# Kernel tuning notes

Measured on AMD Instinct MI355X. Metric: run time of the kernel, lower is better.

Reference implementation:

```python
import jax, jax.numpy as jnp
import numpy as np

# Irreps config: node = 64x0e + 32x1o, edge sh = 1x0e + 1x1o
N, E = 50000, 800000
MUL0, MUL1 = 64, 32
D_IN = MUL0 + 3 * MUL1          # 160
FC_H = 64
W_NUMEL = MUL0 + MUL0 + MUL1 + MUL1  # 192, per-instruction uvu weights
SQRT3 = 1.7320508075688772
ACT_C = 1.6791   # e3nn normalize2mom constant for silu


def setup_inputs() -> dict:
    key = jax.random.key(0)
    ks = jax.random.split(key, 11)
    return {
        "x": jax.random.normal(ks[0], (N, D_IN), jnp.float32),
        "edge_scalars": jax.random.uniform(ks[1], (E, FC_H), dtype=jnp.float32),
        "edge_attr_sh": jax.random.normal(ks[2], (E, 4), jnp.float32),
        "edge_index": jax.random.randint(ks[3], (2, E), 0, N),
        "w_fc1": jax.random.normal(ks[4], (FC_H, FC_H), jnp.float32),
        "w_fc2": jax.random.normal(ks[5], (FC_H, W_NUMEL), jnp.float32),
        "w_sc_s": jax.random.normal(ks[6], (MUL0, MUL0), jnp.float32),
        "w_sc_v": jax.random.normal(ks[7], (MUL1, MUL1), jnp.float32),
        "w_lin_s": jax.random.normal(ks[8], (96, MUL0), jnp.float32),
        "w_lin_v": jax.random.normal(ks[9], (96, MUL1), jnp.float32),
        "w_alpha": jax.random.normal(ks[10], (96, 1), jnp.float32) * 0.1,
    }


def reference(x, edge_scalars, edge_attr_sh, edge_index, w_fc1, w_fc2,
              w_sc_s, w_sc_v, w_lin_s, w_lin_v, w_alpha):
    src, dst = edge_index[0], edge_index[1]

    # --- fc: FullyConnectedNet([64, 64, 192], silu), e3nn fan-in norm ---
    h = jax.nn.silu(edge_scalars @ w_fc1 / np.sqrt(FC_H)) * ACT_C
    weight = h @ w_fc2 / np.sqrt(FC_H)                       # [E, 192]
    w0 = weight[:, :MUL0]                 # 0e x 0e -> 0e (mul 64)
    w1 = weight[:, MUL0:2 * MUL0]         # 0e x 1o -> 1o (mul 64)
    w2 = weight[:, 2 * MUL0:2 * MUL0 + MUL1]   # 1o x 0e -> 1o (mul 32)
    w3 = weight[:, 2 * MUL0 + MUL1:]           # 1o x 1o -> 0e (mul 32)

    # --- self connection: o3.Linear(in -> out), per-irrep mixing ---
    x_s = x[:, :MUL0]                                   # [N, 64]
    x_v = x[:, MUL0:].reshape(N, MUL1, 3)               # [N, 32, 3]
    sc_s = x_s @ w_sc_s / np.sqrt(MUL0)
    sc_v = jnp.einsum('nui,uw->nwi', x_v, w_sc_v) / np.sqrt(MUL1)
    sc_out = jnp.concatenate([sc_s, sc_v.reshape(N, 3 * MUL1)], axis=1)

    # --- gather + edge-weighted uvu tensor product ---
    gx_s = x_s[src]                                     # [E, 64]
    gx_v = x_v[src]                                     # [E, 32, 3]
    sh_s = edge_attr_sh[:, 0:1]                         # [E, 1]
    sh_v = edge_attr_sh[:, 1:4]                         # [E, 3]

    # path weights fold with w3j so factors cancel for 1o outputs
    mid_s0 = w0 * gx_s * sh_s                                        # [E,64] 0e
    mid_s1 = w3 * jnp.einsum('eui,ei->eu', gx_v, sh_v) / SQRT3       # [E,32] 0e
    mid_v0 = w1[:, :, None] * gx_s[:, :, None] * sh_v[:, None, :]    # [E,64,3] 1o
    mid_v1 = w2[:, :, None] * gx_v * sh_s[:, :, None]                # [E,32,3] 1o
    edge_feat = jnp.concatenate(
        [mid_s0, mid_s1, mid_v0.reshape(E, 3 * MUL0), mid_v1.reshape(E, 3 * MUL1)],
        axis=1)                                                      # [E, 384]

    # --- scatter-mean to destination nodes ---
    seg = jax.ops.segment_sum(edge_feat, dst, num_segments=N)
    cnt = jax.ops.segment_sum(jnp.ones((E,), edge_feat.dtype), dst, num_segments=N)
    mean = seg / jnp.maximum(cnt, 1.0)[:, None]                      # [N, 384]

    m_s = mean[:, :96]                                   # 96x0e
    m_v = mean[:, 96:].reshape(N, 96, 3)                 # 96x1o

    # --- alpha gate (o3.Linear mid -> 0e) and output linear ---
    alpha = m_s @ w_alpha / np.sqrt(96)                  # [N, 1]
    lin_s = m_s @ w_lin_s / np.sqrt(96)                  # [N, 64]
    lin_v = jnp.einsum('nui,uw->nwi', m_v, w_lin_v) / np.sqrt(96)
    lin_out = jnp.concatenate([lin_s, lin_v.reshape(N, 3 * MUL1)], axis=1)

    # sc.output_mask is all-ones here (every output irrep reachable)
    return sc_out + alpha * lin_out
```

## Files before the change

### kernel.cpp

```cpp
#include <hip/hip_runtime.h>

#define N_NODES 50000
#define N_EDGES 800000
#define MUL0 64
#define MUL1 32
#define D_IN 160
#define FC_H 64
#define W_NUMEL 192
#define FEAT 384
#define ACT_C 1.6791f
#define INV_SQRT3 0.57735026918962576f
#define RSQRT32 0.17677669529663687f
#define RSQRT96 0.10206207261596575f

#define TILE 32

typedef __attribute__((ext_vector_type(8))) short s16x8;
typedef __attribute__((ext_vector_type(4))) float f32x4;
typedef _Float16 h8 __attribute__((ext_vector_type(8)));
typedef __fp16 fp16x2 __attribute__((ext_vector_type(2)));

static __device__ __forceinline__ unsigned short f2bf(float f) {
    unsigned u = __builtin_bit_cast(unsigned, f);
    unsigned r = (u + 0x7fffu + ((u >> 16) & 1u)) >> 16;
    return (unsigned short)r;
}

static __device__ __forceinline__ int swz(int row, int byte_in_row) {
    int unit = ((row & 1) << 2) | (byte_in_row >> 4);
    int su = unit ^ ((row >> 1) & 7);
    return (row >> 1) * 128 + su * 16 + (byte_in_row & 15);
}
static __device__ __forceinline__ h8 rdh8(const unsigned char* base, int row, int eb) {
    return *(const h8*)(base + swz(row, eb));
}


__global__ __launch_bounds__(256) void hist_kernel(const int* __restrict__ eidx,
                                                   int* __restrict__ cnt) {
    int e = blockIdx.x * 256 + threadIdx.x;
    if (e < N_EDGES) atomicAdd(&cnt[eidx[N_EDGES + e]], 1);
}

#define SCAN_NB 64
#define SCAN_CH ((N_NODES + SCAN_NB - 1) / SCAN_NB)

__global__ __launch_bounds__(256) void scanA_kernel(const int* __restrict__ cnt,
                                                    int* __restrict__ bsum) {
    __shared__ int sred[4];
    int b = blockIdx.x, t = threadIdx.x;
    int lim = min((b + 1) * SCAN_CH, N_NODES);
    int s = 0;
    for (int i = b * SCAN_CH + t; i < lim; i += 256) s += cnt[i];
    for (int d = 1; d < 64; d <<= 1) s += __shfl_xor(s, d);
    if ((t & 63) == 0) sred[t >> 6] = s;
    __syncthreads();
    if (t == 0) bsum[b] = sred[0] + sred[1] + sred[2] + sred[3];
}

__global__ __launch_bounds__(64) void scanB_kernel(const int* __restrict__ bsum,
                                                   int* __restrict__ boff) {
    int t = threadIdx.x;
    int v = bsum[t];
    int p = v;
    for (int d = 1; d < 64; d <<= 1) { int u = __shfl_up(p, d); if (t >= d) p += u; }
    boff[t] = p - v;
}

__global__ __launch_bounds__(256) void scanC_kernel(const int* __restrict__ cnt,
                                                    const int* __restrict__ boff,
                                                    int* __restrict__ fill) {
    __shared__ int s_w[4];
    int b = blockIdx.x, t = threadIdx.x;
    const int CH2 = (SCAN_CH + 255) / 256;
    int base = b * SCAN_CH + t * CH2;
    int lim = min((b + 1) * SCAN_CH, N_NODES);
    int s = 0;
#pragma unroll
    for (int k = 0; k < CH2; ++k) { int i = base + k; if (i < lim) s += cnt[i]; }
    int v = s;
    for (int d = 1; d < 64; d <<= 1) { int u = __shfl_up(v, d); if ((t & 63) >= d) v += u; }
    if ((t & 63) == 63) s_w[t >> 6] = v;
    __syncthreads();
    if (t == 0) { int run = 0; for (int w = 0; w < 4; ++w) { int tv = s_w[w]; s_w[w] = run; run += tv; } }
    __syncthreads();
    int run = boff[b] + s_w[t >> 6] + (v - s);
#pragma unroll
    for (int k = 0; k < CH2; ++k) {
        int i = base + k;
        if (i < lim) { fill[i] = run; run += cnt[i]; }
    }
}

__global__ __launch_bounds__(256) void scatter_ids_kernel(const int* __restrict__ eidx,
                                                          int* __restrict__ fill,
                                                          int* __restrict__ sorted_eid) {
    int e = blockIdx.x * 256 + threadIdx.x;
    if (e < N_EDGES) {
        int p = atomicAdd(&fill[eidx[N_EDGES + e]], 1);
        sorted_eid[p] = e;
    }
}

__global__ __launch_bounds__(256) void prep_w_kernel(
    const float* __restrict__ w_fc1,
    const float* __restrict__ w_fc2,
    const float* __restrict__ w_sc_s,
    const float* __restrict__ w_sc_v,
    const float* __restrict__ w_lin_s,
    const float* __restrict__ w_lin_v,
    unsigned short* __restrict__ w1t,
    unsigned short* __restrict__ w2t,
    unsigned short* __restrict__ wscs_t,
    unsigned short* __restrict__ wscv_t,
    unsigned short* __restrict__ wlins_t,
    unsigned short* __restrict__ wlinv_t)
{
    int i = blockIdx.x * 256 + threadIdx.x;
    if (i < 64 * 64)  w1t[i]    = f2bf(w_fc1[(i & 63) * FC_H + (i >> 6)]);
    if (i < 192 * 64) w2t[i]    = f2bf(w_fc2[(i & 63) * W_NUMEL + (i >> 6)]);
    if (i < 64 * 64)  wscs_t[i] = f2bf(w_sc_s[(i & 63) * 64 + (i >> 6)]);
    if (i < 32 * 32)  wscv_t[i] = f2bf(w_sc_v[(i & 31) * 32 + (i >> 5)]);
    if (i < 64 * 96)  wlins_t[i] = f2bf(w_lin_s[(i % 96) * 64 + (i / 96)]);
    if (i < 32 * 96)  wlinv_t[i] = f2bf(w_lin_v[(i % 96) * 32 + (i / 96)]);
}

#define X_OFF    0
#define W_OFF    10240
#define SH_OFF   22528
#define SID_OFF  22784
#define SEGN_OFF 22848
#define NSEG_OFF 22976
#define SMEM_SZ  22980

static __device__ __forceinline__ h8 seg_mask(const unsigned* vv, unsigned tgt) {
    h8 a;
#pragma unroll
    for (int w2 = 0; w2 < 4; ++w2) {
        a[w2 * 2]     = ((vv[w2] & 0xffffu) == tgt) ? (_Float16)1.f : (_Float16)0.f;
        a[w2 * 2 + 1] = ((vv[w2] >> 16)     == tgt) ? (_Float16)1.f : (_Float16)0.f;
    }
    return a;
}

__global__ __launch_bounds__(256) void edge_kernel(
    const float* __restrict__ x,
    const float* __restrict__ es,
    const float* __restrict__ sh,
    const int*   __restrict__ eidx,
    const int*   __restrict__ sorted_eid,
    const unsigned short* __restrict__ w1t,
    const unsigned short* __restrict__ w2t,
    float* __restrict__ accg)
{
    __shared__ __align__(16) unsigned char smem[SMEM_SZ];
    int* s_segnode = (int*)(smem + SEGN_OFF);
    unsigned short* s_sid = (unsigned short*)(smem + SID_OFF);

    const int t = threadIdx.x;
    const int l = t & 63;
    const int wv = t >> 6;
    const int lr = l & 15;
    const int lk = l >> 4;
    const int rg   = wv & 1;
    const int half = wv >> 1;
    const int tile0 = blockIdx.x * TILE;

    s16x8 w1b[2][2];
#pragma unroll
    for (int j = 0; j < 2; ++j)
#pragma unroll
        for (int kk = 0; kk < 2; ++kk)
            w1b[j][kk] = *(const s16x8*)(w1t + ((half * 2 + j) * 16 + lr) * 64 + kk * 32 + lk * 8);

    int eid_own = sorted_eid[tile0 + rg * 16 + lr];
    float4 esf[4];
    {
        const float4* ep = (const float4*)(es + (size_t)eid_own * FC_H);
        esf[0] = ep[lk * 2];     esf[1] = ep[lk * 2 + 1];
        esf[2] = ep[8 + lk * 2]; esf[3] = ep[8 + lk * 2 + 1];
    }
    const int xe = l & 31;
    const int xc0 = (wv * 2 + (l >> 5)) * 5;
    const int src_e = eidx[sorted_eid[tile0 + xe]];
    float4 xg[5];
    {
        const float4* xp = (const float4*)(x + (size_t)src_e * D_IN);
#pragma unroll
        for (int k = 0; k < 5; ++k) xg[k] = xp[xc0 + k];
    }
    float shv = 0.f;
    if (t < 128) shv = sh[(size_t)sorted_eid[tile0 + (t >> 2)] * 4 + (t & 3)];
    if (wv == 0) {
        int dl = (l < 32) ? eidx[N_EDGES + sorted_eid[tile0 + l]] : -1;
        int nd = __shfl_down(dl, 1);
        bool flag = (l == 31) || (l < 31 && dl != nd);
        unsigned long long m = __ballot(flag) & 0xffffffffull;
        int sid = __popcll(m & ((1ull << l) - 1ull));
        if (l < 32) {
            s_sid[l] = (unsigned short)sid;
            if (flag) s_segnode[sid] = dl;
            if (l == 31) *(int*)(smem + NSEG_OFF) = sid + 1;
        }
    }

    unsigned short* s_h = (unsigned short*)(smem + X_OFF);
    s16x8 afrag[2];
    {
        s16x8 a;
        a[0] = f2bf(esf[0].x); a[1] = f2bf(esf[0].y); a[2] = f2bf(esf[0].z); a[3] = f2bf(esf[0].w);
        a[4] = f2bf(esf[1].x); a[5] = f2bf(esf[1].y); a[6] = f2bf(esf[1].z); a[7] = f2bf(esf[1].w);
        afrag[0] = a;
        a[0] = f2bf(esf[2].x); a[1] = f2bf(esf[2].y); a[2] = f2bf(esf[2].z); a[3] = f2bf(esf[2].w);
        a[4] = f2bf(esf[3].x); a[5] = f2bf(esf[3].y); a[6] = f2bf(esf[3].z); a[7] = f2bf(esf[3].w);
        afrag[1] = a;
    }
#pragma unroll
    for (int j = 0; j < 2; ++j) {
        int nt = half * 2 + j;
        f32x4 hacc = {0.f, 0.f, 0.f, 0.f};
#pragma unroll
        for (int kk = 0; kk < 2; ++kk)
            hacc = __builtin_amdgcn_mfma_f32_16x16x32_bf16(afrag[kk], w1b[j][kk], hacc, 0, 0, 0);
#pragma unroll
        for (int q = 0; q < 4; ++q) {
            float aa = hacc[q] * 0.125f;
            float hv = aa * (1.f / (1.f + __expf(-aa))) * ACT_C;
            s_h[(rg * 16 + lk * 4 + q) * 72 + nt * 16 + lr] = f2bf(hv);
        }
    }
    __syncthreads();

    s16x8 hfrag[2];
#pragma unroll
    for (int kk = 0; kk < 2; ++kk)
        hfrag[kk] = *(const s16x8*)(s_h + (rg * 16 + lr) * 72 + kk * 32 + lk * 8);
    __syncthreads();

#pragma unroll
    for (int j = 0; j < 6; ++j) {
        int nt = half * 6 + j;
        f32x4 acc = {0.f, 0.f, 0.f, 0.f};
#pragma unroll
        for (int kk = 0; kk < 2; ++kk) {
            s16x8 b = *(const s16x8*)(w2t + (nt * 16 + lr) * 64 + kk * 32 + lk * 8);
            acc = __builtin_amdgcn_mfma_f32_16x16x32_bf16(hfrag[kk], b, acc, 0, 0, 0);
        }
        int f = nt * 16 + lr;
        fp16x2 p0 = __builtin_amdgcn_cvt_pkrtz(acc[0] * 0.125f, acc[1] * 0.125f);
        fp16x2 p1 = __builtin_amdgcn_cvt_pkrtz(acc[2] * 0.125f, acc[3] * 0.125f);
        uint2 wval = { __builtin_bit_cast(unsigned, p0), __builtin_bit_cast(unsigned, p1) };
        *(uint2*)(smem + W_OFF + swz(f, rg * 32 + lk * 8)) = wval;
    }
#pragma unroll
    for (int k = 0; k < 5; ++k) {
        float4 v = xg[k];
#pragma unroll
        for (int jj = 0; jj < 4; ++jj) {
            int r = (xc0 + k) * 4 + jj;
            float fv = (jj == 0) ? v.x : (jj == 1) ? v.y : (jj == 2) ? v.z : v.w;
            *(_Float16*)(smem + X_OFF + swz(r, xe * 2)) = (_Float16)fv;
        }
    }
    if (t < 128) {
        int e = t >> 2, c = t & 3;
        *(_Float16*)(smem + SH_OFF + swz(c, e * 2)) = (_Float16)shv;
    }
    __syncthreads();

    const int nseg = *(const int*)(smem + NSEG_OFF);
    const int eb = lk * 16;

    h8 shr[4];
#pragma unroll
    for (int r = 0; r < 4; ++r) shr[r] = rdh8(smem + SH_OFF, r, eb);
    uint4 sv = *(const uint4*)(smem + SID_OFF + eb);
    unsigned vv[4] = { sv.x, sv.y, sv.z, sv.w };

#pragma unroll
    for (int jj = 0; jj < 4; ++jj) {
        const int job = wv * 4 + jj;
        int cls, colbase;
        if (job < 4)       { cls = 0; colbase = job * 16; }
        else if (job < 10) { cls = 1; colbase = (job - 4) * 16; }
        else if (job < 14) { cls = 2; colbase = (job - 10) * 16; }
        else               { cls = 3; colbase = (job - 14) * 16; }
        const int col = colbase + lr;

        h8 B;
        if (cls == 0)      B = rdh8(smem + W_OFF, col, eb)        * rdh8(smem + X_OFF, col, eb);
        else if (cls == 1) B = rdh8(smem + W_OFF, 128 + col / 3, eb) * rdh8(smem + X_OFF, 64 + col, eb);
        else if (cls == 2) B = rdh8(smem + W_OFF, 64 + col, eb)   * rdh8(smem + X_OFF, col, eb);
        else {
            h8 d = rdh8(smem + X_OFF, 64 + 3 * col, eb)     * shr[1]
                 + rdh8(smem + X_OFF, 64 + 3 * col + 1, eb) * shr[2]
                 + rdh8(smem + X_OFF, 64 + 3 * col + 2, eb) * shr[3];
            B = rdh8(smem + W_OFF, 160 + col, eb) * d;
        }

        const int npass = (cls == 2) ? (3 * nseg + 15) >> 4 : (nseg + 15) >> 4;
        for (int p = 0; p < npass; ++p) {
            int m = p * 16 + lr;
            h8 A;
            if (cls == 2) {
                int sg = m / 3, i3 = m - 3 * sg;
                h8 shs = (i3 == 0) ? shr[1] : (i3 == 1) ? shr[2] : shr[3];
                A = seg_mask(vv, (unsigned)sg) * shs;
            } else if (cls == 3) {
                A = seg_mask(vv, (unsigned)m);
            } else {
                A = seg_mask(vv, (unsigned)m) * shr[0];
            }
            f32x4 acc = {0.f, 0.f, 0.f, 0.f};
            acc = __builtin_amdgcn_mfma_f32_16x16x32_f16(A, B, acc, 0, 0, 0);
#pragma unroll
            for (int q = 0; q < 4; ++q) {
                int mrow = p * 16 + lk * 4 + q;
                int sg, f; float sc = 1.f;
                if (cls == 0)      { sg = mrow; f = col; }
                else if (cls == 1) { sg = mrow; f = 288 + col; }
                else if (cls == 2) { sg = mrow / 3; f = 96 + 3 * col + (mrow - 3 * sg); }
                else               { sg = mrow; f = 64 + col; sc = INV_SQRT3; }
                if (sg < nseg) {
                    float val = acc[q] * sc;
                    float* addr = accg + (size_t)s_segnode[sg] * FEAT + f;
                    if (sg > 0 && sg < nseg - 1) *addr = val;
                    else atomicAdd(addr, val);
                }
            }
        }
    }
}


static __device__ __forceinline__ s16x8 frag_c8(const float* p, float s) {
    float4 u = *(const float4*)p, v = *(const float4*)(p + 4);
    s16x8 a;
    a[0] = f2bf(u.x * s); a[1] = f2bf(u.y * s); a[2] = f2bf(u.z * s); a[3] = f2bf(u.w * s);
    a[4] = f2bf(v.x * s); a[5] = f2bf(v.y * s); a[6] = f2bf(v.z * s); a[7] = f2bf(v.w * s);
    return a;
}

__global__ __launch_bounds__(256) void node_kernel(
    const float* __restrict__ x,
    const float* __restrict__ accg,
    const int*   __restrict__ cnt,
    const unsigned short* __restrict__ wscs_t,
    const unsigned short* __restrict__ wscv_t,
    const unsigned short* __restrict__ wlins_t,
    const unsigned short* __restrict__ wlinv_t,
    const float* __restrict__ w_alpha,
    float* __restrict__ out)
{
    const int t = threadIdx.x;
    const int wv = t >> 6, l = t & 63;
    const int lr = l & 15, lk = l >> 4;
    const int n_base = blockIdx.x * 64 + wv * 16;
    const int nrow = n_base + lr;
    const int nclamp = min(nrow, N_NODES - 1);

    const float* mrow = accg + (size_t)nclamp * FEAT;
    const float* xrow = x + (size_t)nclamp * D_IN;
    const float rinv = 1.f / (float)max(cnt[nclamp], 1);

    s16x8 ax[2], ams[3], axv[3], amv[3][3];
#pragma unroll
    for (int kk = 0; kk < 2; ++kk) ax[kk] = frag_c8(xrow + kk * 32 + lk * 8, 1.f);
#pragma unroll
    for (int kk = 0; kk < 3; ++kk) ams[kk] = frag_c8(mrow + kk * 32 + lk * 8, rinv);
    {
        float xb[24];
        const float4* p = (const float4*)(xrow + 64 + 24 * lk);
#pragma unroll
        for (int q = 0; q < 6; ++q) ((float4*)xb)[q] = p[q];
#pragma unroll
        for (int i = 0; i < 3; ++i) {
            s16x8 a;
#pragma unroll
            for (int j = 0; j < 8; ++j) a[j] = f2bf(xb[3 * j + i]);
            axv[i] = a;
        }
    }
#pragma unroll
    for (int kk = 0; kk < 3; ++kk) {
        float mb[24];
        const float4* p = (const float4*)(mrow + 96 + 96 * kk + 24 * lk);
#pragma unroll
        for (int q = 0; q < 6; ++q) ((float4*)mb)[q] = p[q];
#pragma unroll
        for (int i = 0; i < 3; ++i) {
            s16x8 a;
#pragma unroll
            for (int j = 0; j < 8; ++j) a[j] = f2bf(mb[3 * j + i] * rinv);
            amv[i][kk] = a;
        }
    }

    float ap = 0.f;
    {
        float ab[24];
        const float4* p = (const float4*)(mrow + 24 * lk);
#pragma unroll
        for (int q = 0; q < 6; ++q) ((float4*)ab)[q] = p[q];
#pragma unroll
        for (int j = 0; j < 24; ++j) ap += ab[j] * rinv * w_alpha[lk * 24 + j];
    }
    ap += __shfl_xor(ap, 16);
    ap += __shfl_xor(ap, 32);
    const float alphav = ap * RSQRT96;

    f32x4 accA[4], accL[4];
#pragma unroll
    for (int nt = 0; nt < 4; ++nt) { accA[nt] = (f32x4){0,0,0,0}; accL[nt] = (f32x4){0,0,0,0}; }
#pragma unroll
    for (int nt = 0; nt < 4; ++nt) {
#pragma unroll
        for (int kk = 0; kk < 2; ++kk) {
            s16x8 b = *(const s16x8*)(wscs_t + (nt * 16 + lr) * 64 + kk * 32 + lk * 8);
            accA[nt] = __builtin_amdgcn_mfma_f32_16x16x32_bf16(ax[kk], b, accA[nt], 0, 0, 0);
        }
#pragma unroll
        for (int kk = 0; kk < 3; ++kk) {
            s16x8 b = *(const s16x8*)(wlins_t + (nt * 16 + lr) * 96 + kk * 32 + lk * 8);
            accL[nt] = __builtin_amdgcn_mfma_f32_16x16x32_bf16(ams[kk], b, accL[nt], 0, 0, 0);
        }
    }
    f32x4 accVs[3][2], accVl[3][2];
#pragma unroll
    for (int i = 0; i < 3; ++i)
#pragma unroll
        for (int nt = 0; nt < 2; ++nt) { accVs[i][nt] = (f32x4){0,0,0,0}; accVl[i][nt] = (f32x4){0,0,0,0}; }
#pragma unroll
    for (int i = 0; i < 3; ++i) {
#pragma unroll
        for (int nt = 0; nt < 2; ++nt) {
            s16x8 b = *(const s16x8*)(wscv_t + (nt * 16 + lr) * 32 + lk * 8);
            accVs[i][nt] = __builtin_amdgcn_mfma_f32_16x16x32_bf16(axv[i], b, accVs[i][nt], 0, 0, 0);
#pragma unroll
            for (int kk = 0; kk < 3; ++kk) {
                s16x8 b2 = *(const s16x8*)(wlinv_t + (nt * 16 + lr) * 96 + kk * 32 + lk * 8);
                accVl[i][nt] = __builtin_amdgcn_mfma_f32_16x16x32_bf16(amv[i][kk], b2, accVl[i][nt], 0, 0, 0);
            }
        }
    }

#pragma unroll
    for (int q = 0; q < 4; ++q) {
        int row = lk * 4 + q;
        float ar = __shfl(alphav, row);
        int n = n_base + row;
        bool ok = (n < N_NODES);
        float* orow = out + (size_t)n * 160;
#pragma unroll
        for (int nt = 0; nt < 4; ++nt) {
            float vout = accA[nt][q] * 0.125f + ar * accL[nt][q] * RSQRT96;
            if (ok) orow[nt * 16 + lr] = vout;
        }
#pragma unroll
        for (int i = 0; i < 3; ++i)
#pragma unroll
            for (int nt = 0; nt < 2; ++nt) {
                float vout = accVs[i][nt][q] * RSQRT32 + ar * accVl[i][nt][q] * RSQRT96;
                if (ok) orow[64 + 3 * (nt * 16 + lr) + i] = vout;
            }
    }
}


extern "C" void kernel_launch(void* const* d_in, const int* in_sizes, int n_in,
                              void* d_out, int out_size, void* d_ws, size_t ws_size,
                              hipStream_t stream) {
    const float* x        = (const float*)d_in[0];
    const float* es       = (const float*)d_in[1];
    const float* sh       = (const float*)d_in[2];
    const int*   eidx     = (const int*)d_in[3];
    const float* w_fc1    = (const float*)d_in[4];
    const float* w_fc2    = (const float*)d_in[5];
    const float* w_sc_s   = (const float*)d_in[6];
    const float* w_sc_v   = (const float*)d_in[7];
    const float* w_lin_s  = (const float*)d_in[8];
    const float* w_lin_v  = (const float*)d_in[9];
    const float* w_alpha  = (const float*)d_in[10];
    float* out = (float*)d_out;

    float* accg       = (float*)d_ws;
    int*   cnt        = (int*)(accg + (size_t)N_NODES * FEAT);
    int*   fill       = cnt + N_NODES;
    int*   sorted_eid = fill + N_NODES;
    unsigned short* w1t     = (unsigned short*)(sorted_eid + N_EDGES);
    unsigned short* w2t     = w1t + 64 * 64;
    unsigned short* wscs_t  = w2t + 192 * 64;
    unsigned short* wscv_t  = wscs_t + 64 * 64;
    unsigned short* wlins_t = wscv_t + 32 * 32;
    unsigned short* wlinv_t = wlins_t + 64 * 96;
    int* bsum = (int*)(wlinv_t + 32 * 96);
    int* boff = bsum + SCAN_NB;

    (void)hipMemsetAsync(d_ws, 0, ((size_t)N_NODES * FEAT + N_NODES) * 4, stream);
    hipLaunchKernelGGL(hist_kernel, dim3((N_EDGES + 255) / 256), dim3(256), 0, stream,
                       eidx, cnt);
    hipLaunchKernelGGL(scanA_kernel, dim3(SCAN_NB), dim3(256), 0, stream, cnt, bsum);
    hipLaunchKernelGGL(scanB_kernel, dim3(1), dim3(64), 0, stream, bsum, boff);
    hipLaunchKernelGGL(scanC_kernel, dim3(SCAN_NB), dim3(256), 0, stream, cnt, boff, fill);
    hipLaunchKernelGGL(scatter_ids_kernel, dim3((N_EDGES + 255) / 256), dim3(256), 0, stream,
                       eidx, fill, sorted_eid);
    hipLaunchKernelGGL(prep_w_kernel, dim3(48), dim3(256), 0, stream,
                       w_fc1, w_fc2, w_sc_s, w_sc_v, w_lin_s, w_lin_v,
                       w1t, w2t, wscs_t, wscv_t, wlins_t, wlinv_t);
    hipLaunchKernelGGL(edge_kernel, dim3(N_EDGES / TILE), dim3(256), 0, stream,
                       x, es, sh, eidx, sorted_eid, w1t, w2t, accg);
    hipLaunchKernelGGL(node_kernel, dim3((N_NODES + 63) / 64), dim3(256), 0, stream,
                       x, accg, cnt, wscs_t, wscv_t, wlins_t, wlinv_t, w_alpha, out);
}
```

Baseline: 483.3 us.

## Regroup edge-kernel MFMA jobs per wave to share A fragments and row addressing

Reassigns the 16 column jobs so each wave handles jobs of one segment-row shape. This lets it build the segment mask / A operand and the per-row node pointers once per pass and reuse them across four MFMAs, instead of recomputing them per job. The class-3 jobs (which use the unscaled mask) are moved into wave 2 alongside class-1 jobs, and the 3x-row class-2 work gets its own wave. The change also swaps the manual float-to-bf16 rounding for the HIP intrinsic. The trade-off is more live registers and a possibly unbalanced workload, since wave 3 does three times as many passes.

After: 475.1 us. About the same (-1.7%).

```diff
diff --git a/kernel.cpp b/kernel.cpp
--- a/kernel.cpp
+++ b/kernel.cpp
@@ -1,4 +1,5 @@
 #include <hip/hip_runtime.h>
+#include <hip/hip_bf16.h>
 
 #define N_NODES 50000
 #define N_EDGES 800000
@@ -21,9 +22,8 @@
 typedef __fp16 fp16x2 __attribute__((ext_vector_type(2)));
 
 static __device__ __forceinline__ unsigned short f2bf(float f) {
-    unsigned u = __builtin_bit_cast(unsigned, f);
-    unsigned r = (u + 0x7fffu + ((u >> 16) & 1u)) >> 16;
-    return (unsigned short)r;
+    __hip_bfloat16 b = __float2bfloat16(f);
+    return __builtin_bit_cast(unsigned short, b);
 }
 
 static __device__ __forceinline__ int swz(int row, int byte_in_row) {
@@ -271,61 +271,114 @@
     const int nseg = *(const int*)(smem + NSEG_OFF);
     const int eb = lk * 16;
 
-    h8 shr[4];
-#pragma unroll
-    for (int r = 0; r < 4; ++r) shr[r] = rdh8(smem + SH_OFF, r, eb);
+    h8 shreg[4];
+#pragma unroll
+    for (int r = 0; r < 4; ++r) shreg[r] = rdh8(smem + SH_OFF, r, eb);
     uint4 sv = *(const uint4*)(smem + SID_OFF + eb);
     unsigned vv[4] = { sv.x, sv.y, sv.z, sv.w };
 
-#pragma unroll
-    for (int jj = 0; jj < 4; ++jj) {
-        const int job = wv * 4 + jj;
-        int cls, colbase;
-        if (job < 4)       { cls = 0; colbase = job * 16; }
-        else if (job < 10) { cls = 1; colbase = (job - 4) * 16; }
-        else if (job < 14) { cls = 2; colbase = (job - 10) * 16; }
-        else               { cls = 3; colbase = (job - 14) * 16; }
-        const int col = colbase + lr;
-
-        h8 B;
-        if (cls == 0)      B = rdh8(smem + W_OFF, col, eb)        * rdh8(smem + X_OFF, col, eb);
-        else if (cls == 1) B = rdh8(smem + W_OFF, 128 + col / 3, eb) * rdh8(smem + X_OFF, 64 + col, eb);
-        else if (cls == 2) B = rdh8(smem + W_OFF, 64 + col, eb)   * rdh8(smem + X_OFF, col, eb);
-        else {
-            h8 d = rdh8(smem + X_OFF, 64 + 3 * col, eb)     * shr[1]
-                 + rdh8(smem + X_OFF, 64 + 3 * col + 1, eb) * shr[2]
-                 + rdh8(smem + X_OFF, 64 + 3 * col + 2, eb) * shr[3];
-            B = rdh8(smem + W_OFF, 160 + col, eb) * d;
-        }
-
-        const int npass = (cls == 2) ? (3 * nseg + 15) >> 4 : (nseg + 15) >> 4;
+    h8 Bv[4];
+    int fcol[4];
+    bool cls3j[4] = {false, false, false, false};
+    if (wv == 0) {
+#pragma unroll
+        for (int jj = 0; jj < 4; ++jj) {
+            int col = jj * 16 + lr;
+            Bv[jj] = rdh8(smem + W_OFF, col, eb) * rdh8(smem + X_OFF, col, eb);
+            fcol[jj] = col;
+        }
+    } else if (wv == 1) {
+#pragma unroll
+        for (int jj = 0; jj < 4; ++jj) {
+            int col = jj * 16 + lr;
+            Bv[jj] = rdh8(smem + W_OFF, 128 + col / 3, eb) * rdh8(smem + X_OFF, 64 + col, eb);
+            fcol[jj] = 288 + col;
+        }
+    } else if (wv == 2) {
+#pragma unroll
+        for (int jj = 0; jj < 2; ++jj) {
+            int col = 64 + jj * 16 + lr;
+            Bv[jj] = rdh8(smem + W_OFF, 128 + col / 3, eb) * rdh8(smem + X_OFF, 64 + col, eb);
+            fcol[jj] = 288 + col;
+        }
+#pragma unroll
+        for (int jj = 2; jj < 4; ++jj) {
+            int col = (jj - 2) * 16 + lr;
+            h8 d = rdh8(smem + X_OFF, 64 + 3 * col, eb)     * shreg[1]
+                 + rdh8(smem + X_OFF, 64 + 3 * col + 1, eb) * shreg[2]
+                 + rdh8(smem + X_OFF, 64 + 3 * col + 2, eb) * shreg[3];
+            Bv[jj] = rdh8(smem + W_OFF, 160 + col, eb) * d;
+            fcol[jj] = 64 + col;
+            cls3j[jj] = true;
+        }
+    } else {
+#pragma unroll
+        for (int jj = 0; jj < 4; ++jj) {
+            int col = jj * 16 + lr;
+            Bv[jj] = rdh8(smem + W_OFF, 64 + col, eb) * rdh8(smem + X_OFF, col, eb);
+            fcol[jj] = 96 + 3 * col;
+        }
+    }
+
+    if (wv != 3) {
+        const int npass = (nseg + 15) >> 4;
+        for (int p = 0; p < npass; ++p) {
+            h8 bm = seg_mask(vv, (unsigned)(p * 16 + lr));
+            h8 Ash = bm * shreg[0];
+            const int m0 = p * 16 + lk * 4;
+            float* nptr[4]; bool valid[4], atq[4];
+#pragma unroll
+            for (int q = 0; q < 4; ++q) {
+                int sg = m0 + q;
+                valid[q] = sg < nseg;
+                int node = valid[q] ? s_segnode[sg] : 0;
+                nptr[q] = accg + (size_t)node * FEAT;
+                atq[q] = (sg == 0) || (sg == nseg - 1);
+            }
+#pragma unroll
+            for (int jj = 0; jj < 4; ++jj) {
+                f32x4 acc = {0.f, 0.f, 0.f, 0.f};
+                acc = __builtin_amdgcn_mfma_f32_16x16x32_f16(cls3j[jj] ? bm : Ash, Bv[jj], acc, 0, 0, 0);
+                const float sc = cls3j[jj] ? INV_SQRT3 : 1.f;
+#pragma unroll
+                for (int q = 0; q < 4; ++q) {
+                    if (valid[q]) {
+                        float v = acc[q] * sc;
+                        float* a = nptr[q] + fcol[jj];
+                        if (atq[q]) atomicAdd(a, v); else *a = v;
+                    }
+                }
+            }
+        }
+    } else {
+        const int npass = (3 * nseg + 15) >> 4;
         for (int p = 0; p < npass; ++p) {
             int m = p * 16 + lr;
-            h8 A;
-            if (cls == 2) {
-                int sg = m / 3, i3 = m - 3 * sg;
-                h8 shs = (i3 == 0) ? shr[1] : (i3 == 1) ? shr[2] : shr[3];
-                A = seg_mask(vv, (unsigned)sg) * shs;
-            } else if (cls == 3) {
-                A = seg_mask(vv, (unsigned)m);
-            } else {
-                A = seg_mask(vv, (unsigned)m) * shr[0];
+            int sgA = m / 3, i3A = m - 3 * sgA;
+            h8 A = seg_mask(vv, (unsigned)sgA) *
+                   ((i3A == 0) ? shreg[1] : (i3A == 1) ? shreg[2] : shreg[3]);
+            int m0 = p * 16 + lk * 4;
+            int sgq = m0 / 3, rq = m0 - 3 * sgq;
+            float* nptr[4]; int i3q[4]; bool valid[4], atq[4];
+#pragma unroll
+            for (int q = 0; q < 4; ++q) {
+                valid[q] = sgq < nseg;
+                int node = valid[q] ? s_segnode[sgq] : 0;
+                nptr[q] = accg + (size_t)node * FEAT;
+                i3q[q] = rq;
+                atq[q] = (sgq == 0) || (sgq == nseg - 1);
+                if (++rq == 3) { rq = 0; ++sgq; }
             }
-            f32x4 acc = {0.f, 0.f, 0.f, 0.f};
-            acc = __builtin_amdgcn_mfma_f32_16x16x32_f16(A, B, acc, 0, 0, 0);
-#pragma unroll
-            for (int q = 0; q < 4; ++q) {
-                int mrow = p * 16 + lk * 4 + q;
-                int sg, f; float sc = 1.f;
-                if (cls == 0)      { sg = mrow; f = col; }
-                else if (cls == 1) { sg = mrow; f = 288 + col; }
-                else if (cls == 2) { sg = mrow / 3; f = 96 + 3 * col + (mrow - 3 * sg); }
-                else               { sg = mrow; f = 64 + col; sc = INV_SQRT3; }
-                if (sg < nseg) {
-                    float val = acc[q] * sc;
-                    float* addr = accg + (size_t)s_segnode[sg] * FEAT + f;
-                    if (sg > 0 && sg < nseg - 1) *addr = val;
-                    else atomicAdd(addr, val);
+#pragma unroll
+            for (int jj = 0; jj < 4; ++jj) {
+                f32x4 acc = {0.f, 0.f, 0.f, 0.f};
+                acc = __builtin_amdgcn_mfma_f32_16x16x32_f16(A, Bv[jj], acc, 0, 0, 0);
+#pragma unroll
+                for (int q = 0; q < 4; ++q) {
+                    if (valid[q]) {
+                        float* a = nptr[q] + fcol[jj] + i3q[q];
+                        if (atq[q]) atomicAdd(a, acc[q]); else *a = acc[q];
+                    }
                 }
             }
         }
```
